# Kernel optimization log

Measured on AMD Instinct MI355X. Metric: run time of the kernel, lower is better.

Reference implementation:

```python
import jax, jax.numpy as jnp
import numpy as np


def setup_inputs() -> dict:
    key = jax.random.key(0)
    k1, k2 = jax.random.split(key)
    B, C, H, W = 16, 128, 128, 128
    x = jax.random.normal(k1, (B, C, H, W), dtype=jnp.float32)
    # 1x1 conv weight, no bias: [out_channels, in_channels]
    w = jax.random.normal(k2, (C, C), dtype=jnp.float32) * (1.0 / np.sqrt(C))
    return {"x": x, "w": w}


def reference(x, w):
    # x: [B, C, H, W]; original computes y = x @ (x^T x) / (H*W) over flattened
    # spatial dim N = H*W, then a 1x1 conv. We reassociate exactly:
    #   x @ (x^T x) == (x x^T) @ x   (associativity of matmul)
    # avoiding the O(N^2) intermediate; math is identical.
    B, C, H, W = x.shape
    N = H * W
    xf = x.reshape(B, C, N)                              # [B, C, N]
    gram = jnp.einsum('bcn,bdn->bcd', xf, xf) / N        # [B, C, C] = (x x^T)/N
    y = jnp.einsum('bcd,bdn->bcn', gram, xf)             # [B, C, N]
    y = y.reshape(B, C, H, W)
    # 1x1 conv (bias=False) == per-pixel channel mixing
    out = jnp.einsum('oc,bchw->bohw', w, y)              # [B, C, H, W]
    return out
```

## Files before the change

kernel.cpp:

```cpp
#include <hip/hip_runtime.h>

typedef __attribute__((ext_vector_type(8))) short bf16x8;
typedef __attribute__((ext_vector_type(4))) float f32x4;
typedef __attribute__((ext_vector_type(4))) float f4v;

#define NB 16
#define NC 128
#define NN 16384

__device__ __forceinline__ unsigned int f2bf_pack(float lo, float hi) {
  unsigned int ulo = __float_as_uint(lo);
  unsigned int uhi = __float_as_uint(hi);
  ulo = (ulo + 0x7FFFu + ((ulo >> 16) & 1u)) >> 16;
  uhi = (uhi + 0x7FFFu + ((uhi >> 16) & 1u)) & 0xFFFF0000u;
  return ulo | uhi;
}

__global__ __launch_bounds__(256, 2)
void nlm_gram_kernel(const float* __restrict__ x, float* __restrict__ partials,
                     int chunks, int ksteps) {
  __shared__ __align__(16) char lds[2 * 128 * 64 * 2];
  const int t = threadIdx.x;
  const int b  = blockIdx.x / chunks;
  const int ch = blockIdx.x % chunks;
  const int lane = t & 63, wv = t >> 6, l15 = lane & 15, q = lane >> 4;
  const int kc = ksteps * 64;

  const float* xb = x + (size_t)b * NC * NN + (size_t)ch * kc;

  f32x4 acc[2][8];
#pragma unroll
  for (int i = 0; i < 2; ++i)
#pragma unroll
    for (int j = 0; j < 8; ++j) acc[i][j] = (f32x4){0.f, 0.f, 0.f, 0.f};

  int srow[4], sseg[4];
#pragma unroll
  for (int i = 0; i < 4; ++i) { int id = t + 256 * i; srow[i] = id >> 3; sseg[i] = id & 7; }

  f4v pfA[4][2], pfB[4][2];

#define LOADPF(PF, KS)                                                      \
  {                                                                         \
    _Pragma("unroll") for (int i = 0; i < 4; ++i) {                         \
      const float* src = xb + (size_t)srow[i] * NN + (KS)*64 + sseg[i] * 8; \
      PF[i][0] = *(const f4v*)src;                                          \
      PF[i][1] = *(const f4v*)(src + 4);                                    \
    }                                                                       \
  }

#define PACKPF(PF, BUF)                                                     \
  {                                                                         \
    _Pragma("unroll") for (int i = 0; i < 4; ++i) {                         \
      uint4 pk;                                                             \
      pk.x = f2bf_pack(PF[i][0][0], PF[i][0][1]);                           \
      pk.y = f2bf_pack(PF[i][0][2], PF[i][0][3]);                           \
      pk.z = f2bf_pack(PF[i][1][0], PF[i][1][1]);                           \
      pk.w = f2bf_pack(PF[i][1][2], PF[i][1][3]);                           \
      int byte = (srow[i] * 128 + sseg[i] * 16) ^ ((srow[i] & 7) << 4);     \
      *(uint4*)((BUF) + byte) = pk;                                         \
    }                                                                       \
  }

#define MFMAPH(BUF)                                                                          \
  {                                                                                          \
    _Pragma("unroll") for (int kh = 0; kh < 2; ++kh) {                                       \
      const int kbyte = kh * 64 + q * 16;                                                    \
      int ra = wv * 32 + l15;                                                                \
      bf16x8 a0 = *(const bf16x8*)((BUF) + ((ra * 128 + kbyte) ^ ((ra & 7) << 4)));          \
      int rb = wv * 32 + 16 + l15;                                                           \
      bf16x8 a1 = *(const bf16x8*)((BUF) + ((rb * 128 + kbyte) ^ ((rb & 7) << 4)));          \
      _Pragma("unroll") for (int ct = 0; ct < 8; ++ct) {                                     \
        int rc = ct * 16 + l15;                                                              \
        bf16x8 bb = *(const bf16x8*)((BUF) + ((rc * 128 + kbyte) ^ ((rc & 7) << 4)));        \
        acc[0][ct] = __builtin_amdgcn_mfma_f32_16x16x32_bf16(a0, bb, acc[0][ct], 0, 0, 0);   \
        acc[1][ct] = __builtin_amdgcn_mfma_f32_16x16x32_bf16(a1, bb, acc[1][ct], 0, 0, 0);   \
      }                                                                                      \
    }                                                                                        \
  }

  char* buf0 = lds;
  char* buf1 = lds + 16384;

  LOADPF(pfA, 0);
  PACKPF(pfA, buf0);
  if (1 < ksteps) LOADPF(pfB, 1);
  __syncthreads();

  for (int ks = 0; ks < ksteps; ks += 2) {
    if (ks + 2 < ksteps) LOADPF(pfA, ks + 2);
    MFMAPH(buf0);
    if (ks + 1 < ksteps) PACKPF(pfB, buf1);
    __syncthreads();
    if (ks + 1 < ksteps) {
      if (ks + 3 < ksteps) LOADPF(pfB, ks + 3);
      MFMAPH(buf1);
      if (ks + 2 < ksteps) PACKPF(pfA, buf0);
      __syncthreads();
    }
  }

  float* part = partials + (size_t)blockIdx.x * (NC * NC);
#pragma unroll
  for (int rt = 0; rt < 2; ++rt)
#pragma unroll
    for (int ct = 0; ct < 8; ++ct)
#pragma unroll
      for (int r = 0; r < 4; ++r) {
        int i = wv * 32 + rt * 16 + q * 4 + r;
        int j = ct * 16 + l15;
        part[i * 128 + j] = acc[rt][ct][r];
      }
#undef LOADPF
#undef PACKPF
#undef MFMAPH
}

__global__ __launch_bounds__(256)
void nlm_gramw_kernel(const float* __restrict__ partials, const float* __restrict__ w,
                      unsigned short* __restrict__ Mbf, int chunks) {
  __shared__ __align__(16) float glds[8 * 128];
  const int t = threadIdx.x;
  const int b  = blockIdx.x >> 4;
  const int d0 = (blockIdx.x & 15) * 8;

  const int rr = t >> 5;
  const int c4 = (t & 31) * 4;
  const float* pb = partials + (size_t)b * chunks * (NC * NC) + (d0 + rr) * 128 + c4;
  f4v s = (f4v){0.f, 0.f, 0.f, 0.f};
  for (int chn = 0; chn < chunks; ++chn)
    s += *(const f4v*)(pb + (size_t)chn * (NC * NC));
  s *= (1.0f / 16384.0f);
  *(f4v*)(glds + rr * 128 + c4) = s;
  __syncthreads();

  const int o  = t & 127;
  const int j0 = (t >> 7) * 4;
  float m[4] = {0.f, 0.f, 0.f, 0.f};
  for (int c = 0; c < 128; c += 4) {
    f4v wv = *(const f4v*)(w + o * 128 + c);
#pragma unroll
    for (int j = 0; j < 4; ++j) {
      f4v gv = *(const f4v*)(glds + (j0 + j) * 128 + c);
      m[j] = fmaf(wv[0], gv[0], m[j]);
      m[j] = fmaf(wv[1], gv[1], m[j]);
      m[j] = fmaf(wv[2], gv[2], m[j]);
      m[j] = fmaf(wv[3], gv[3], m[j]);
    }
  }
  uint2 pk;
  pk.x = f2bf_pack(m[0], m[1]);
  pk.y = f2bf_pack(m[2], m[3]);
  *(uint2*)(Mbf + (size_t)b * NC * NC + o * 128 + d0 + j0) = pk;
}

__global__ __launch_bounds__(256, 2)
void nlm_out_kernel(const float* __restrict__ x, const unsigned short* __restrict__ Mbf,
                    float* __restrict__ out) {
  __shared__ __align__(16) char lds[128 * 128 * 2];
  const int t = threadIdx.x;
  const int b = blockIdx.x >> 7;
  const int n0 = (blockIdx.x & 127) * 128;
  const int lane = t & 63, wv = t >> 6, l15 = lane & 15, q = lane >> 4;

  bf16x8 afr[2][4];
  const unsigned short* mb = Mbf + (size_t)b * NC * NC;
#pragma unroll
  for (int rt = 0; rt < 2; ++rt)
#pragma unroll
    for (int ks = 0; ks < 4; ++ks) {
      int o = wv * 32 + rt * 16 + l15;
      afr[rt][ks] = *(const bf16x8*)(mb + o * 128 + ks * 32 + q * 8);
    }

  const float* xb = x + (size_t)b * NC * NN + n0;
#pragma unroll
  for (int i = 0; i < 2; ++i) {
    int id = t + 256 * i;
    int nb = id & 31, cb = id >> 5;
    const float* src = xb + (size_t)(cb * 8) * NN + nb * 4;
    f4v v[8];
#pragma unroll
    for (int r = 0; r < 8; ++r) v[r] = *(const f4v*)(src + (size_t)r * NN);
#pragma unroll
    for (int j = 0; j < 4; ++j) {
      int n = nb * 4 + j;
      uint4 pk;
      pk.x = f2bf_pack(v[0][j], v[1][j]);
      pk.y = f2bf_pack(v[2][j], v[3][j]);
      pk.z = f2bf_pack(v[4][j], v[5][j]);
      pk.w = f2bf_pack(v[6][j], v[7][j]);
      int byte = (n * 256 + cb * 16) ^ ((((n & 7) ^ ((n >> 3) & 7))) << 4);
      *(uint4*)(lds + byte) = pk;
    }
  }
  __syncthreads();

  f32x4 acc[2][8];
#pragma unroll
  for (int i = 0; i < 2; ++i)
#pragma unroll
    for (int j = 0; j < 8; ++j) acc[i][j] = (f32x4){0.f, 0.f, 0.f, 0.f};

#pragma unroll
  for (int ks = 0; ks < 4; ++ks) {
#pragma unroll
    for (int ct = 0; ct < 8; ++ct) {
      int n = ct * 16 + l15;
      int byte = (n * 256 + ks * 64 + q * 16) ^ ((((n & 7) ^ ((n >> 3) & 7))) << 4);
      bf16x8 bfr = *(const bf16x8*)(lds + byte);
      acc[0][ct] = __builtin_amdgcn_mfma_f32_16x16x32_bf16(afr[0][ks], bfr, acc[0][ct], 0, 0, 0);
      acc[1][ct] = __builtin_amdgcn_mfma_f32_16x16x32_bf16(afr[1][ks], bfr, acc[1][ct], 0, 0, 0);
    }
  }

  float* ob = out + (size_t)b * NC * NN + n0;
#pragma unroll
  for (int rt = 0; rt < 2; ++rt)
#pragma unroll
    for (int ct = 0; ct < 8; ++ct)
#pragma unroll
      for (int r = 0; r < 4; ++r) {
        int o = wv * 32 + rt * 16 + q * 4 + r;
        int n = ct * 16 + l15;
        ob[(size_t)o * NN + n] = acc[rt][ct][r];
      }
}

extern "C" void kernel_launch(void* const* d_in, const int* in_sizes, int n_in,
                              void* d_out, int out_size, void* d_ws, size_t ws_size,
                              hipStream_t stream) {
  const float* x = (const float*)d_in[0];
  const float* w = (const float*)d_in[1];
  float* out = (float*)d_out;

  int chunks = 32;
  while (chunks > 1 &&
         (size_t)NB * chunks * NC * NC * sizeof(float) +
         (size_t)NB * NC * NC * 2 > ws_size)
    chunks >>= 1;
  int ksteps = (NN / chunks) / 64;

  char* wsp = (char*)d_ws;
  float* partials = (float*)wsp;
  wsp += (size_t)NB * chunks * NC * NC * sizeof(float);
  unsigned short* Mbf = (unsigned short*)wsp;

  hipLaunchKernelGGL(nlm_gram_kernel, dim3(NB * chunks), dim3(256), 0, stream,
                     x, partials, chunks, ksteps);
  hipLaunchKernelGGL(nlm_gramw_kernel, dim3(NB * 16), dim3(256), 0, stream,
                     partials, w, Mbf, chunks);
  hipLaunchKernelGGL(nlm_out_kernel, dim3(NB * 128), dim3(256), 0, stream,
                     x, Mbf, out);
}
```

Baseline: 88.28 us.

## Store Gram partials in bf16 and reverse batch order in output kernel

```diff
diff --git a/kernel.cpp b/kernel.cpp
--- a/kernel.cpp
+++ b/kernel.cpp
@@ -3,6 +3,7 @@
 typedef __attribute__((ext_vector_type(8))) short bf16x8;
 typedef __attribute__((ext_vector_type(4))) float f32x4;
 typedef __attribute__((ext_vector_type(4))) float f4v;
+typedef __attribute__((ext_vector_type(4))) unsigned short u16x4;
 
 #define NB 16
 #define NC 128
@@ -16,8 +17,17 @@
   return ulo | uhi;
 }
 
+__device__ __forceinline__ unsigned short f2bf_one(float v) {
+  unsigned int u = __float_as_uint(v);
+  return (unsigned short)((u + 0x7FFFu + ((u >> 16) & 1u)) >> 16);
+}
+
+__device__ __forceinline__ float bf2f(unsigned short u) {
+  return __uint_as_float(((unsigned int)u) << 16);
+}
+
 __global__ __launch_bounds__(256, 2)
-void nlm_gram_kernel(const float* __restrict__ x, float* __restrict__ partials,
+void nlm_gram_kernel(const float* __restrict__ x, unsigned short* __restrict__ partials,
                      int chunks, int ksteps) {
   __shared__ __align__(16) char lds[2 * 128 * 64 * 2];
   const int t = threadIdx.x;
@@ -100,7 +110,7 @@
     }
   }
 
-  float* part = partials + (size_t)blockIdx.x * (NC * NC);
+  unsigned short* part = partials + (size_t)blockIdx.x * (NC * NC);
 #pragma unroll
   for (int rt = 0; rt < 2; ++rt)
 #pragma unroll
@@ -109,7 +119,7 @@
       for (int r = 0; r < 4; ++r) {
         int i = wv * 32 + rt * 16 + q * 4 + r;
         int j = ct * 16 + l15;
-        part[i * 128 + j] = acc[rt][ct][r];
+        part[i * 128 + j] = f2bf_one(acc[rt][ct][r]);
       }
 #undef LOADPF
 #undef PACKPF
@@ -117,7 +127,7 @@
 }
 
 __global__ __launch_bounds__(256)
-void nlm_gramw_kernel(const float* __restrict__ partials, const float* __restrict__ w,
+void nlm_gramw_kernel(const unsigned short* __restrict__ partials, const float* __restrict__ w,
                       unsigned short* __restrict__ Mbf, int chunks) {
   __shared__ __align__(16) float glds[8 * 128];
   const int t = threadIdx.x;
@@ -126,10 +136,16 @@
 
   const int rr = t >> 5;
   const int c4 = (t & 31) * 4;
-  const float* pb = partials + (size_t)b * chunks * (NC * NC) + (d0 + rr) * 128 + c4;
+  const unsigned short* pb =
+      partials + (size_t)b * chunks * (NC * NC) + (d0 + rr) * 128 + c4;
   f4v s = (f4v){0.f, 0.f, 0.f, 0.f};
-  for (int chn = 0; chn < chunks; ++chn)
-    s += *(const f4v*)(pb + (size_t)chn * (NC * NC));
+  for (int chn = 0; chn < chunks; ++chn) {
+    u16x4 v = *(const u16x4*)(pb + (size_t)chn * (NC * NC));
+    s[0] += bf2f(v[0]);
+    s[1] += bf2f(v[1]);
+    s[2] += bf2f(v[2]);
+    s[3] += bf2f(v[3]);
+  }
   s *= (1.0f / 16384.0f);
   *(f4v*)(glds + rr * 128 + c4) = s;
   __syncthreads();
@@ -159,7 +175,7 @@
                     float* __restrict__ out) {
   __shared__ __align__(16) char lds[128 * 128 * 2];
   const int t = threadIdx.x;
-  const int b = blockIdx.x >> 7;
+  const int b = (NB - 1) - (blockIdx.x >> 7);
   const int n0 = (blockIdx.x & 127) * 128;
   const int lane = t & 63, wv = t >> 6, l15 = lane & 15, q = lane >> 4;
 
@@ -236,14 +252,14 @@
 
   int chunks = 32;
   while (chunks > 1 &&
-         (size_t)NB * chunks * NC * NC * sizeof(float) +
+         (size_t)NB * chunks * NC * NC * 2 +
          (size_t)NB * NC * NC * 2 > ws_size)
     chunks >>= 1;
   int ksteps = (NN / chunks) / 64;
 
   char* wsp = (char*)d_ws;
-  float* partials = (float*)wsp;
-  wsp += (size_t)NB * chunks * NC * NC * sizeof(float);
+  unsigned short* partials = (unsigned short*)wsp;
+  wsp += (size_t)NB * chunks * NC * NC * 2;
   unsigned short* Mbf = (unsigned short*)wsp;
 
   hipLaunchKernelGGL(nlm_gram_kernel, dim3(NB * chunks), dim3(256), 0, stream,
```

After: 88.26 us. Within noise of the previous version (-0.0%).
